# Optimization experiments

Measured on AMD Instinct MI355X. Metric: run time of the kernel, lower is better.

Reference implementation:

```python
import jax, jax.numpy as jnp
import numpy as np
import math

B, T, D, M, V = 16, 256, 256, 32, 50257
EPS = 1e-6


def setup_inputs() -> dict:
    key = jax.random.key(0)
    ks = jax.random.split(key, 24)
    s = 0.02
    inp = {
        'hidden_state': jax.random.normal(ks[0], (B, 2, D), jnp.float32),
        'output_sequence': jax.random.randint(ks[1], (B, T), 0, V),
        # embedding table for output tokens
        'emb_out': jax.random.normal(ks[2], (V, D), jnp.float32) * s,
        # decoder_attention (Wq,Wk,Wv are torch Linear weights [out,in], plus biases)
        'Wq1': jax.random.normal(ks[3], (D, D), jnp.float32) * s,
        'bq1': jnp.zeros((D,), jnp.float32),
        'Wk1': jax.random.normal(ks[4], (D, D), jnp.float32) * s,
        'bk1': jnp.zeros((D,), jnp.float32),
        'Wv1': jax.random.normal(ks[5], (D, D), jnp.float32) * s,
        'bv1': jnp.zeros((D,), jnp.float32),
        # decoder_attention_2
        'Wq2': jax.random.normal(ks[6], (D, D), jnp.float32) * s,
        'bq2': jnp.zeros((D,), jnp.float32),
        'Wk2': jax.random.normal(ks[7], (D, D), jnp.float32) * s,
        'bk2': jnp.zeros((D,), jnp.float32),
        'Wv2': jax.random.normal(ks[8], (D, D), jnp.float32) * s,
        'bv2': jnp.zeros((D,), jnp.float32),
        # decoder_mover / decoder_mover_2 weights: nn.Linear(D, M).weight -> [M, D]
        'mover1': jax.random.normal(ks[9], (M, D), jnp.float32) * s,
        'mover2': jax.random.normal(ks[10], (M, D), jnp.float32) * s,
        # norm2
        'gamma': jnp.ones((D,), jnp.float32),
        'beta': jnp.zeros((D,), jnp.float32),
        # vocab logits linear [V, D] + bias
        'Wvoc': jax.random.normal(ks[11], (V, D), jnp.float32) * s,
        'bvoc': jnp.zeros((V,), jnp.float32),
    }
    return inp


def _attn(q, kv, Wq, bq, Wk, bk, Wv, bv):
    # q: [B,1,D], kv: [B,M+1,D]
    Q = q @ Wq.T + bq
    K = kv @ Wk.T + bk
    Vv = kv @ Wv.T + bv
    s = jnp.einsum('bqd,bkd->bqk', Q, K) / jnp.sqrt(jnp.asarray(Q.shape[-1], Q.dtype))
    a = jax.nn.softmax(s, axis=-1)
    return jnp.einsum('bqk,bkd->bqd', a, Vv)


def _layernorm(x, gamma, beta):
    mu = jnp.mean(x, axis=-1, keepdims=True)
    var = jnp.mean((x - mu) ** 2, axis=-1, keepdims=True)
    return (x - mu) * jax.lax.rsqrt(var + EPS) * gamma + beta


def reference(hidden_state, output_sequence, emb_out,
              Wq1, bq1, Wk1, bk1, Wv1, bv1,
              Wq2, bq2, Wk2, bk2, Wv2, bv2,
              mover1, mover2, gamma, beta, Wvoc, bvoc):
    d = emb_out.shape[1]
    # Embeddings: lookup scaled by sqrt(d) (standard simple-transformer embedding)
    x = emb_out[output_sequence] * jnp.sqrt(jnp.asarray(d, jnp.float32))  # [B,T,D]
    z0 = hidden_state[:, 0:1, :]
    z1 = hidden_state[:, 1:2, :]
    b = z0.shape[0]
    mv1 = jnp.broadcast_to(mover1[None], (b, mover1.shape[0], d))  # static per step
    mv2 = jnp.broadcast_to(mover2[None], (b, mover2.shape[0], d))

    def step(carry, xt):
        z0, z1 = carry
        z0 = z0 + xt[:, None, :]
        g = jnp.concatenate([z0, mv1], axis=1)          # [B,M+1,D]
        dg = _attn(g[:, :1], g, Wq1, bq1, Wk1, bk1, Wv1, bv1)
        g2 = jnp.concatenate([z1, mv2], axis=1)
        dg2 = _attn(g2[:, :1], g2, Wq2, bq2, Wk2, bk2, Wv2, bv2)
        z0 = _layernorm(z0 + dg + dg2, gamma, beta)
        return (z0, z0), None

    (z0, z1), _ = jax.lax.scan(step, (z0, z1), jnp.swapaxes(x, 0, 1))
    logits = z0 @ Wvoc.T + bvoc                         # [B,1,V]
    y = jax.nn.log_softmax(logits, axis=-1)
    return jnp.concatenate([z0, z1], axis=1), y
```

## Files before the change

### kernel.cpp

```cpp
#include <hip/hip_runtime.h>

typedef unsigned int u32;
typedef unsigned short u16;

#define DD 256
#define TT 256
#define MM 32
#define NBATCH 16
#define VV 50257

#define WS_FLAG   0
#define WS_KV     16
#define WS_A      32784
#define WS_W12S   163856
#define WS_CB     180240
#define WS_E12    180752
#define WS_CST    180816
#define WS_ZFIN   180832
#define WS_SSUM   184928
#define WS_WPK    184944
#define WS_US     332400
#define WS_SYNC   369264

#if defined(__has_builtin)
#if __has_builtin(__builtin_amdgcn_fdot2)
#define HAS_FDOT2 1
#endif
#endif

typedef _Float16 half2_t __attribute__((ext_vector_type(2)));

__device__ __forceinline__ float bf2f(u16 v){ return __uint_as_float(((u32)v) << 16); }
__device__ __forceinline__ float ldf(const void* p, size_t i, int bf){
  return bf ? bf2f(((const u16*)p)[i]) : ((const float*)p)[i];
}
__device__ __forceinline__ u32 packh2(float a, float b){
  union { half2_t h; u32 u; } x;
  x.h[0] = (_Float16)a; x.h[1] = (_Float16)b;
  return x.u;
}
__device__ __forceinline__ float fdot2(u32 a, u32 b, float c){
  union { u32 u; half2_t h; } ua, ub;
  ua.u = a; ub.u = b;
#ifdef HAS_FDOT2
  return __builtin_amdgcn_fdot2(ua.h, ub.h, c, false);
#else
  return c + (float)ua.h[0]*(float)ub.h[0] + (float)ua.h[1]*(float)ub.h[1];
#endif
}
__device__ __forceinline__ u32 ldu(const u32* p){
  return __hip_atomic_load(p, __ATOMIC_RELAXED, __HIP_MEMORY_SCOPE_SYSTEM);
}
__device__ __forceinline__ void stu(u32* p, u32 v){
  __hip_atomic_store(p, v, __ATOMIC_RELAXED, __HIP_MEMORY_SCOPE_SYSTEM);
}
__device__ __forceinline__ void stv_tag(float* p, float v, u32 tag){
  stu((u32*)p, (__float_as_uint(v) & ~1u) | tag);
}

__global__ __launch_bounds__(256) void k_init(const u32* gam, u32* flag,
                                              float* Ssum, u32* sync, u32* usg){
  const int gtid = blockIdx.x*256 + threadIdx.x;
  if (blockIdx.x == 0){
    if (threadIdx.x == 0) *flag = (gam[0] == 0x3F800000u) ? 0u : 1u;
    if (threadIdx.x < 16) Ssum[threadIdx.x] = 0.f;
    for (int i = threadIdx.x; i < 512; i += 256) sync[i] = 0u;
  }
  for (int i = gtid; i < NBATCH*2304; i += 8*256) stu(&usg[i], 1u);
}

__global__ __launch_bounds__(256) void k_prep1(
  const void* Wk1, const void* bk1, const void* Wv1, const void* bv1,
  const void* Wk2, const void* bk2, const void* Wv2, const void* bv2,
  const void* m1, const void* m2, float* KV, const u32* flagp)
{
  const int bf = (int)*flagp;
  int mat = blockIdx.x >> 5, j = blockIdx.x & 31, d = threadIdx.x;
  const void *W, *bias, *mv;
  if (mat == 0){ W = Wk1; bias = bk1; mv = m1; }
  else if (mat == 1){ W = Wv1; bias = bv1; mv = m1; }
  else if (mat == 2){ W = Wk2; bias = bk2; mv = m2; }
  else { W = Wv2; bias = bv2; mv = m2; }
  float acc = ldf(bias, d, bf);
  for (int e = 0; e < DD; ++e) acc += ldf(W, d*DD + e, bf) * ldf(mv, j*DD + e, bf);
  KV[mat*8192 + j*DD + d] = acc;
}

__global__ __launch_bounds__(256) void k_prep2(
  const void* Wq1, const void* Wk1, const void* bq1, const void* bk1,
  const void* Wq2, const void* Wk2, const void* bq2, const void* bk2,
  const float* KV, float* A, float* W12s, float* cb, float* e12, float* cst,
  const u32* flagp)
{
  const int bf = (int)*flagp;
  int blk = blockIdx.x, tid = threadIdx.x;
  if (blk < 512){
    int mat = blk >> 8, i = blk & 255;
    const void* Wq = mat ? Wq2 : Wq1;
    const void* Wk = mat ? Wk2 : Wk1;
    float acc = 0.f;
    for (int e = 0; e < DD; ++e) acc += ldf(Wq, e*DD + i, bf) * ldf(Wk, e*DD + tid, bf);
    A[mat*65536 + i*DD + tid] = acc;
  } else if (blk < 576){
    int idx = blk - 512, mat = idx >> 5, j = idx & 31;
    const void* Wq = mat ? Wq2 : Wq1;
    const float* K = KV + mat*16384;
    float acc = 0.f;
    for (int e = 0; e < DD; ++e) acc += ldf(Wq, e*DD + tid, bf) * K[j*DD + e];
    W12s[mat*8192 + j*DD + tid] = acc;
  } else if (blk < 578){
    int mat = blk - 576;
    const void* Wq = mat ? Wq2 : Wq1;
    const void* Wk = mat ? Wk2 : Wk1;
    const void* bq = mat ? bq2 : bq1;
    const void* bk = mat ? bk2 : bk1;
    float acc = 0.f;
    for (int e = 0; e < DD; ++e)
      acc += ldf(Wk, e*DD + tid, bf) * ldf(bq, e, bf) + ldf(Wq, e*DD + tid, bf) * ldf(bk, e, bf);
    cb[mat*DD + tid] = acc;
  } else {
    if (tid < 32){
      float acc = 0.f;
      for (int d = 0; d < DD; ++d) acc += ldf(bq1, d, bf) * KV[tid*DD + d];
      e12[tid] = acc;
    } else if (tid < 64){
      int j = tid - 32; float acc = 0.f;
      for (int d = 0; d < DD; ++d) acc += ldf(bq2, d, bf) * KV[16384 + j*DD + d];
      e12[32 + j] = acc;
    } else if (tid == 64){
      float acc = 0.f;
      for (int d = 0; d < DD; ++d) acc += ldf(bq1, d, bf) * ldf(bk1, d, bf);
      cst[0] = acc;
    } else if (tid == 65){
      float acc = 0.f;
      for (int d = 0; d < DD; ++d) acc += ldf(bq2, d, bf) * ldf(bk2, d, bf);
      cst[1] = acc;
    }
  }
}

__global__ __launch_bounds__(256) void k_pack(
  const float* __restrict__ A, const float* __restrict__ W12s,
  const float* __restrict__ cb, const void* __restrict__ Wv1,
  const void* __restrict__ Wv2, u32* __restrict__ Wpk, const u32* flagp)
{
  const int bf = (int)*flagp;
  int idx = blockIdx.x*256 + threadIdx.x;
  float v0 = 0.f, v1 = 0.f;
  if (idx < 131072){
    int p = idx >> 15;
    int r2 = idx & 32767;
    int e2g = r2 >> 10;
    int t = (r2 >> 2) & 255;
    int q = r2 & 3;
    int c = e2g*8 + q*2;
    if (p == 0){ v0 = A[t*DD + c]; v1 = A[t*DD + c + 1]; }
    else if (p == 1){ v0 = ldf(Wv1, t*DD + c, bf); v1 = ldf(Wv1, t*DD + c + 1, bf); }
    else if (p == 2){ v0 = A[65536 + t*DD + c]; v1 = A[65536 + t*DD + c + 1]; }
    else { v0 = ldf(Wv2, t*DD + c, bf); v1 = ldf(Wv2, t*DD + c + 1, bf); }
  } else {
    int rem = idx - 131072;
    int t = rem >> 7;
    int e2g = (rem >> 2) & 31;
    int q = rem & 3;
    int c = e2g*8 + q*2;
    if (t < 32){ v0 = W12s[t*DD + c]; v1 = W12s[t*DD + c + 1]; }
    else if (t < 64){ v0 = W12s[8192 + (t-32)*DD + c]; v1 = W12s[8192 + (t-32)*DD + c + 1]; }
    else if (t == 64){ v0 = cb[c]; v1 = cb[c + 1]; }
    else if (t == 65){ v0 = cb[DD + c]; v1 = cb[DD + c + 1]; }
  }
  Wpk[idx] = packh2(v0, v1);
}

__global__ __launch_bounds__(256) void k_seq(
    const void* __restrict__ hid, const int* __restrict__ seq,
    const void* __restrict__ emb,
    const u32* __restrict__ Wpk, const float* __restrict__ V1g,
    const float* __restrict__ V2g, const float* __restrict__ e1g,
    const float* __restrict__ e2g_, const float* __restrict__ cst,
    const void* __restrict__ bv1, const void* __restrict__ bv2,
    const void* __restrict__ gam, const void* __restrict__ bet,
    float* __restrict__ zfin, float* __restrict__ out0,
    const u32* __restrict__ flagp, float* __restrict__ usg,
    u32* __restrict__ syncg)
{
  (void)syncg;
  __shared__ float z0s[DD], z1s[DD];
  __shared__ __align__(16) u32 zp0[128], zp1[128];
  __shared__ u32 V1h[MM*DD/2], V2h[MM*DD/2];
  __shared__ float a1s[33], a2s[33];
  __shared__ float red[16];
  __shared__ float gs[DD], bs[DD], bv1s[DD], bv2s[DD];
  __shared__ float e1s[MM], e2s[MM];
  __shared__ int toks[TT];

  const int tid = threadIdx.x;
  const int wg = blockIdx.x;
  const int b = wg >> 2;
  const int g = wg & 3;
  const int lane = tid & 63;
  const int wv = tid >> 6;
  const int bf = (int)*flagp;

  float* us0 = usg + b*2304;
  float* us1 = us0 + 1152;

  for (int r = tid; r < MM*DD/2; r += 256){
    V1h[r] = packh2(V1g[2*r], V1g[2*r + 1]);
    V2h[r] = packh2(V2g[2*r], V2g[2*r + 1]);
  }
  for (int r = tid; r < TT; r += 256) toks[r] = seq[b*TT + r];
  gs[tid] = ldf(gam, tid, bf); bs[tid] = ldf(bet, tid, bf);
  bv1s[tid] = ldf(bv1, tid, bf); bv2s[tid] = ldf(bv2, tid, bf);
  if (tid < MM){ e1s[tid] = e1g[tid]; e2s[tid] = e2g_[tid]; }
  const float c1 = cst[0], c2 = cst[1];
  __syncthreads();
  z1s[tid] = ldf(hid, b*2*DD + DD + tid, bf);
  z0s[tid] = ldf(hid, b*2*DD + tid, bf) + ldf(emb, (size_t)toks[0]*DD + tid, bf) * 16.0f;
  __syncthreads();

  const uint4* Wp = (const uint4*)Wpk;
  const uint4* wpMain = Wp + g*8192 + tid;
  const int p4row = g*32 + (tid >> 3);
  const uint4* wpP4 = Wp + 32768 + p4row*32 + (tid & 7);
  const bool p4z1 = (p4row >= 32 && p4row < 64) || (p4row == 65);

  int xi;
  if (tid < 2) xi = 1088 + tid;
  else if (tid >= 64 && tid < 128) xi = 1024 + (tid - 64);
  else xi = tid;

  for (int t = 0; t < TT; ++t){
    float* usw = (t & 1) ? us1 : us0;
    const u32 tg = (u32)((t >> 1) & 1);
    float xnext = 0.f;
    if (t + 1 < TT) xnext = ldf(emb, (size_t)toks[t+1]*DD + tid, bf) * 16.0f;

    if (tid < 128) zp0[tid] = packh2(z0s[2*tid], z0s[2*tid+1]);
    else { int i = tid - 128; zp1[i] = packh2(z1s[2*i], z1s[2*i+1]); }
    __syncthreads();

    {
      const uint4* zp4 = (const uint4*)((g < 2) ? zp0 : zp1);
      float a0 = 0.f, a1 = 0.f, a2 = 0.f, a3 = 0.f;
      #pragma unroll 8
      for (int k = 0; k < 32; ++k){
        uint4 w = wpMain[k*256];
        uint4 z = zp4[k];
        a0 = fdot2(w.x, z.x, a0);
        a1 = fdot2(w.y, z.y, a1);
        a2 = fdot2(w.z, z.z, a2);
        a3 = fdot2(w.w, z.w, a3);
      }
      stv_tag(&usw[g*256 + tid], (a0 + a1) + (a2 + a3), tg);
    }
    {
      const uint4* zq = (const uint4*)(p4z1 ? zp1 : zp0);
      float a0 = 0.f, a1 = 0.f, a2 = 0.f, a3 = 0.f;
      #pragma unroll
      for (int j = 0; j < 4; ++j){
        uint4 w = wpP4[j*8];
        uint4 z = zq[(tid & 7) + 8*j];
        a0 = fdot2(w.x, z.x, a0);
        a1 = fdot2(w.y, z.y, a1);
        a2 = fdot2(w.z, z.z, a2);
        a3 = fdot2(w.w, z.w, a3);
      }
      float s = (a0 + a1) + (a2 + a3);
      s += __shfl_down(s, 4, 64);
      s += __shfl_down(s, 2, 64);
      s += __shfl_down(s, 1, 64);
      if ((tid & 7) == 0) stv_tag(&usw[1024 + p4row], s, tg);
    }

    u32 b0, b1, b2, b3, bx;
    {
      const u32* up = (const u32*)usw;
      for (;;){
        b0 = ldu(up + tid);
        b1 = ldu(up + 256 + tid);
        b2 = ldu(up + 512 + tid);
        b3 = ldu(up + 768 + tid);
        bx = ldu(up + xi);
        if ((((b0 ^ tg) | (b1 ^ tg) | (b2 ^ tg) | (b3 ^ tg) | (bx ^ tg)) & 1u) == 0u)
          break;
      }
    }
    float u0  = __uint_as_float(b0);
    float uv1 = __uint_as_float(b1);
    float u2  = __uint_as_float(b2);
    float uv2 = __uint_as_float(b3);
    float xf  = __uint_as_float(bx);

    float p1 = z0s[tid] * u0;
    float p2 = z1s[tid] * u2;
    #pragma unroll
    for (int off = 32; off; off >>= 1){
      p1 += __shfl_down(p1, off, 64);
      p2 += __shfl_down(p2, off, 64);
    }
    if (lane == 0){ red[wv] = p1; red[4 + wv] = p2; }
    __syncthreads();
    if (tid == 0) a1s[0] = (red[0]+red[1]+red[2]+red[3] + xf + c1) * 0.0625f;
    if (tid == 1) a2s[0] = (red[4]+red[5]+red[6]+red[7] + xf + c2) * 0.0625f;
    if (tid >= 64 && tid < 96)  a1s[tid - 63] = (xf + e1s[tid-64]) * 0.0625f;
    if (tid >= 96 && tid < 128) a2s[tid - 95] = (xf + e2s[tid-96]) * 0.0625f;
    __syncthreads();

    if (tid < 128){
      float* sm = (tid < 64) ? a1s : a2s;
      float v = (lane < 33) ? sm[lane] : -1e30f;
      float mx = v;
      #pragma unroll
      for (int off = 32; off; off >>= 1) mx = fmaxf(mx, __shfl_xor(mx, off, 64));
      float e = (lane < 33) ? expf(v - mx) : 0.f;
      float s = e;
      #pragma unroll
      for (int off = 32; off; off >>= 1) s += __shfl_xor(s, off, 64);
      if (lane < 33) sm[lane] = e / s;
    }
    __syncthreads();

    float hv1 = uv1 + bv1s[tid];
    float hv2 = uv2 + bv2s[tid];
    float dg = a1s[0] * hv1;
    float dh = a2s[0] * hv2;
    int half_idx = tid >> 1;
    #pragma unroll
    for (int j = 1; j <= 32; ++j){
      union { u32 u; half2_t h; } pv1, pv2;
      pv1.u = V1h[((j-1) << 7) + half_idx];
      pv2.u = V2h[((j-1) << 7) + half_idx];
      float e1v = (tid & 1) ? (float)pv1.h[1] : (float)pv1.h[0];
      float e2v = (tid & 1) ? (float)pv2.h[1] : (float)pv2.h[0];
      dg += a1s[j] * e1v;
      dh += a2s[j] * e2v;
    }
    float y = z0s[tid] + dg + dh;
    float sy = y, syy = y * y;
    #pragma unroll
    for (int off = 32; off; off >>= 1){
      sy += __shfl_down(sy, off, 64);
      syy += __shfl_down(syy, off, 64);
    }
    if (lane == 0){ red[8 + wv] = sy; red[12 + wv] = syy; }
    __syncthreads();
    float Sy = red[8] + red[9] + red[10] + red[11];
    float Syy = red[12] + red[13] + red[14] + red[15];
    float mu = Sy * (1.f/DD);
    float var = Syy * (1.f/DD) - mu*mu;
    float zi = (y - mu) * rsqrtf(var + 1e-6f) * gs[tid] + bs[tid];
    if (t == TT - 1){
      if (g == 0){
        zfin[b*DD + tid] = zi;
        out0[b*2*DD + tid] = zi;
        out0[b*2*DD + DD + tid] = zi;
      }
    } else {
      z1s[tid] = zi;
      z0s[tid] = zi + xnext;
    }
    __syncthreads();
  }
}

__global__ __launch_bounds__(256) void k_logits(
    const float* __restrict__ zfin, const void* __restrict__ Wvoc,
    const void* __restrict__ bvoc, float* __restrict__ Ssum,
    float* __restrict__ out1, const u32* __restrict__ flagp)
{
  __shared__ float zfs[NBATCH][DD];
  const int tid = threadIdx.x;
  const int bf = (int)*flagp;
  for (int r = tid; r < NBATCH*DD; r += 256) zfs[r >> 8][r & 255] = zfin[r];
  __syncthreads();

  const int v = blockIdx.x*256 + tid;
  float acc[NBATCH];
  const bool ok = (v < VV);
  float bias = ok ? ldf(bvoc, v, bf) : 0.f;
  #pragma unroll
  for (int b = 0; b < NBATCH; ++b) acc[b] = bias;

  if (ok){
    if (bf){
      const uint4* wr = ((const uint4*)Wvoc) + (size_t)v*32;
      for (int gg = 0; gg < 32; ++gg){
        uint4 u = wr[gg];
        float w0 = __uint_as_float(u.x << 16), w1 = __uint_as_float(u.x & 0xffff0000u);
        float w2 = __uint_as_float(u.y << 16), w3 = __uint_as_float(u.y & 0xffff0000u);
        float w4 = __uint_as_float(u.z << 16), w5 = __uint_as_float(u.z & 0xffff0000u);
        float w6 = __uint_as_float(u.w << 16), w7 = __uint_as_float(u.w & 0xffff0000u);
        const int c = gg*8;
        #pragma unroll
        for (int b = 0; b < NBATCH; ++b){
          const float* zc = &zfs[b][c];
          acc[b] += w0*zc[0] + w1*zc[1] + w2*zc[2] + w3*zc[3]
                  + w4*zc[4] + w5*zc[5] + w6*zc[6] + w7*zc[7];
        }
      }
    } else {
      const float4* wr = ((const float4*)Wvoc) + (size_t)v*64;
      for (int gg = 0; gg < 64; ++gg){
        float4 u = wr[gg];
        const int c = gg*4;
        #pragma unroll
        for (int b = 0; b < NBATCH; ++b){
          const float* zc = &zfs[b][c];
          acc[b] += u.x*zc[0] + u.y*zc[1] + u.z*zc[2] + u.w*zc[3];
        }
      }
    }
    #pragma unroll
    for (int b = 0; b < NBATCH; ++b) out1[(size_t)b*VV + v] = acc[b];
  }

  #pragma unroll
  for (int b = 0; b < NBATCH; ++b){
    float p = ok ? expf(acc[b]) : 0.f;
    #pragma unroll
    for (int off = 32; off; off >>= 1) p += __shfl_down(p, off, 64);
    if ((tid & 63) == 0) atomicAdd(&Ssum[b], p);
  }
}

__global__ __launch_bounds__(256) void k_final(
    const float* __restrict__ Ssum, float* __restrict__ out1)
{
  const int v = blockIdx.x*256 + threadIdx.x;
  const int b = blockIdx.y;
  if (v < VV){
    float ls = logf(Ssum[b]);
    size_t i = (size_t)b*VV + v;
    out1[i] = out1[i] - ls;
  }
}

extern "C" void kernel_launch(void* const* d_in, const int* in_sizes, int n_in,
                              void* d_out, int out_size, void* d_ws, size_t ws_size,
                              hipStream_t stream)
{
  (void)in_sizes; (void)n_in; (void)out_size; (void)ws_size;
  const void* hid  = d_in[0];
  const int*  seq  = (const int*)d_in[1];
  const void* emb  = d_in[2];
  const void* Wq1  = d_in[3];
  const void* bq1  = d_in[4];
  const void* Wk1  = d_in[5];
  const void* bk1  = d_in[6];
  const void* Wv1  = d_in[7];
  const void* bv1  = d_in[8];
  const void* Wq2  = d_in[9];
  const void* bq2  = d_in[10];
  const void* Wk2  = d_in[11];
  const void* bk2  = d_in[12];
  const void* Wv2  = d_in[13];
  const void* bv2  = d_in[14];
  const void* m1   = d_in[15];
  const void* m2   = d_in[16];
  const void* gam  = d_in[17];
  const void* bet  = d_in[18];
  const void* Wvoc = d_in[19];
  const void* bvoc = d_in[20];

  float* wsf    = (float*)d_ws;
  u32*   flag   = (u32*)(wsf + WS_FLAG);
  float* KV     = wsf + WS_KV;
  float* A      = wsf + WS_A;
  float* W12s   = wsf + WS_W12S;
  float* cb     = wsf + WS_CB;
  float* e12    = wsf + WS_E12;
  float* cst    = wsf + WS_CST;
  float* zfin   = wsf + WS_ZFIN;
  float* Ssum   = wsf + WS_SSUM;
  u32*   Wpk    = (u32*)(wsf + WS_WPK);
  float* usg    = wsf + WS_US;
  u32*   syncg  = (u32*)(wsf + WS_SYNC);

  float* out0 = (float*)d_out;
  float* out1 = out0 + NBATCH*2*DD;

  k_init<<<8, 256, 0, stream>>>((const u32*)gam, flag, Ssum, syncg, (u32*)usg);
  k_prep1<<<128, 256, 0, stream>>>(Wk1,bk1,Wv1,bv1,Wk2,bk2,Wv2,bv2,m1,m2,KV,flag);
  k_prep2<<<579, 256, 0, stream>>>(Wq1,Wk1,bq1,bk1,Wq2,Wk2,bq2,bk2,KV,A,W12s,cb,e12,cst,flag);
  k_pack<<<576, 256, 0, stream>>>(A,W12s,cb,Wv1,Wv2,Wpk,flag);
  k_seq<<<NBATCH*4, 256, 0, stream>>>(hid, seq, emb, Wpk, KV+8192, KV+24576,
                                      e12, e12+32, cst, bv1, bv2, gam, bet, zfin, out0,
                                      flag, usg, syncg);
  k_logits<<<197, 256, 0, stream>>>(zfin, Wvoc, bvoc, Ssum, out1, flag);
  k_final<<<dim3(197, NBATCH), 256, 0, stream>>>(Ssum, out1);
}
```

Measured before the change: 1.788 ms.

## Map batch groups to same XCD and use agent-scope atomics when co-located

Reorders the block-to-(batch,group) mapping so the four cooperating workgroups of a batch are blockIdx b, b+16, b+32, b+48, which with round-robin XCD dispatch likely places them on the same XCD. At startup each group reads its XCC_ID via s_getreg and publishes it. If all four match, the per-step exchange of tagged partial results uses agent-scope rather than system-scope atomic loads and stores, which is meant to cut the cost of cross-workgroup handoffs in the 256-step sequential loop. It adds a startup handshake and relies on the hardware dispatch order. It also stores a sentinel into the exchange buffers after the loop, and sync is now zeroed with system-scope stores.

```diff
diff --git a/kernel.cpp b/kernel.cpp
--- a/kernel.cpp
+++ b/kernel.cpp
@@ -48,14 +48,26 @@
   return c + (float)ua.h[0]*(float)ub.h[0] + (float)ua.h[1]*(float)ub.h[1];
 #endif
 }
+
 __device__ __forceinline__ u32 ldu(const u32* p){
   return __hip_atomic_load(p, __ATOMIC_RELAXED, __HIP_MEMORY_SCOPE_SYSTEM);
 }
 __device__ __forceinline__ void stu(u32* p, u32 v){
   __hip_atomic_store(p, v, __ATOMIC_RELAXED, __HIP_MEMORY_SCOPE_SYSTEM);
 }
-__device__ __forceinline__ void stv_tag(float* p, float v, u32 tag){
-  stu((u32*)p, (__float_as_uint(v) & ~1u) | tag);
+template<bool FAST>
+__device__ __forceinline__ u32 ldx(const u32* p){
+  return __hip_atomic_load(p, __ATOMIC_RELAXED,
+      FAST ? __HIP_MEMORY_SCOPE_AGENT : __HIP_MEMORY_SCOPE_SYSTEM);
+}
+template<bool FAST>
+__device__ __forceinline__ void stx(u32* p, u32 v){
+  __hip_atomic_store(p, v, __ATOMIC_RELAXED,
+      FAST ? __HIP_MEMORY_SCOPE_AGENT : __HIP_MEMORY_SCOPE_SYSTEM);
+}
+template<bool FAST>
+__device__ __forceinline__ void stx_tag(float* p, float v, u32 tag){
+  stx<FAST>((u32*)p, (__float_as_uint(v) & ~1u) | tag);
 }
 
 __global__ __launch_bounds__(256) void k_init(const u32* gam, u32* flag,
@@ -64,7 +76,7 @@
   if (blockIdx.x == 0){
     if (threadIdx.x == 0) *flag = (gam[0] == 0x3F800000u) ? 0u : 1u;
     if (threadIdx.x < 16) Ssum[threadIdx.x] = 0.f;
-    for (int i = threadIdx.x; i < 512; i += 256) sync[i] = 0u;
+    for (int i = threadIdx.x; i < 512; i += 256) stu(&sync[i], 0u);
   }
   for (int i = gtid; i < NBATCH*2304; i += 8*256) stu(&usg[i], 1u);
 }
@@ -172,64 +184,19 @@
   Wpk[idx] = packh2(v0, v1);
 }
 
-__global__ __launch_bounds__(256) void k_seq(
-    const void* __restrict__ hid, const int* __restrict__ seq,
-    const void* __restrict__ emb,
-    const u32* __restrict__ Wpk, const float* __restrict__ V1g,
-    const float* __restrict__ V2g, const float* __restrict__ e1g,
-    const float* __restrict__ e2g_, const float* __restrict__ cst,
-    const void* __restrict__ bv1, const void* __restrict__ bv2,
-    const void* __restrict__ gam, const void* __restrict__ bet,
-    float* __restrict__ zfin, float* __restrict__ out0,
-    const u32* __restrict__ flagp, float* __restrict__ usg,
-    u32* __restrict__ syncg)
-{
-  (void)syncg;
-  __shared__ float z0s[DD], z1s[DD];
-  __shared__ __align__(16) u32 zp0[128], zp1[128];
-  __shared__ u32 V1h[MM*DD/2], V2h[MM*DD/2];
-  __shared__ float a1s[33], a2s[33];
-  __shared__ float red[16];
-  __shared__ float gs[DD], bs[DD], bv1s[DD], bv2s[DD];
-  __shared__ float e1s[MM], e2s[MM];
-  __shared__ int toks[TT];
-
-  const int tid = threadIdx.x;
-  const int wg = blockIdx.x;
-  const int b = wg >> 2;
-  const int g = wg & 3;
-  const int lane = tid & 63;
-  const int wv = tid >> 6;
-  const int bf = (int)*flagp;
-
-  float* us0 = usg + b*2304;
-  float* us1 = us0 + 1152;
-
-  for (int r = tid; r < MM*DD/2; r += 256){
-    V1h[r] = packh2(V1g[2*r], V1g[2*r + 1]);
-    V2h[r] = packh2(V2g[2*r], V2g[2*r + 1]);
-  }
-  for (int r = tid; r < TT; r += 256) toks[r] = seq[b*TT + r];
-  gs[tid] = ldf(gam, tid, bf); bs[tid] = ldf(bet, tid, bf);
-  bv1s[tid] = ldf(bv1, tid, bf); bv2s[tid] = ldf(bv2, tid, bf);
-  if (tid < MM){ e1s[tid] = e1g[tid]; e2s[tid] = e2g_[tid]; }
-  const float c1 = cst[0], c2 = cst[1];
-  __syncthreads();
-  z1s[tid] = ldf(hid, b*2*DD + DD + tid, bf);
-  z0s[tid] = ldf(hid, b*2*DD + tid, bf) + ldf(emb, (size_t)toks[0]*DD + tid, bf) * 16.0f;
-  __syncthreads();
-
-  const uint4* Wp = (const uint4*)Wpk;
-  const uint4* wpMain = Wp + g*8192 + tid;
-  const int p4row = g*32 + (tid >> 3);
-  const uint4* wpP4 = Wp + 32768 + p4row*32 + (tid & 7);
-  const bool p4z1 = (p4row >= 32 && p4row < 64) || (p4row == 65);
-
-  int xi;
-  if (tid < 2) xi = 1088 + tid;
-  else if (tid >= 64 && tid < 128) xi = 1024 + (tid - 64);
-  else xi = tid;
-
+template<bool FAST>
+__device__ __forceinline__ void seq_loop(
+    int tid, int g, int b, int lane, int wv, int bf,
+    float* us0, float* us1,
+    const uint4* wpMain, const uint4* wpP4, bool p4z1, int p4row, int xi,
+    const void* emb, const int* toks, float c1, float c2,
+    float* z0s, float* z1s, u32* zp0, u32* zp1,
+    const u32* V1h, const u32* V2h,
+    float* a1s, float* a2s, float* red,
+    const float* gs, const float* bs, const float* bv1s, const float* bv2s,
+    const float* e1s, const float* e2s,
+    float* zfin, float* out0)
+{
   for (int t = 0; t < TT; ++t){
     float* usw = (t & 1) ? us1 : us0;
     const u32 tg = (u32)((t >> 1) & 1);
@@ -252,7 +219,7 @@
         a2 = fdot2(w.z, z.z, a2);
         a3 = fdot2(w.w, z.w, a3);
       }
-      stv_tag(&usw[g*256 + tid], (a0 + a1) + (a2 + a3), tg);
+      stx_tag<FAST>(&usw[g*256 + tid], (a0 + a1) + (a2 + a3), tg);
     }
     {
       const uint4* zq = (const uint4*)(p4z1 ? zp1 : zp0);
@@ -270,18 +237,18 @@
       s += __shfl_down(s, 4, 64);
       s += __shfl_down(s, 2, 64);
       s += __shfl_down(s, 1, 64);
-      if ((tid & 7) == 0) stv_tag(&usw[1024 + p4row], s, tg);
+      if ((tid & 7) == 0) stx_tag<FAST>(&usw[1024 + p4row], s, tg);
     }
 
     u32 b0, b1, b2, b3, bx;
     {
       const u32* up = (const u32*)usw;
       for (;;){
-        b0 = ldu(up + tid);
-        b1 = ldu(up + 256 + tid);
-        b2 = ldu(up + 512 + tid);
-        b3 = ldu(up + 768 + tid);
-        bx = ldu(up + xi);
+        b0 = ldx<FAST>(up + tid);
+        b1 = ldx<FAST>(up + 256 + tid);
+        b2 = ldx<FAST>(up + 512 + tid);
+        b3 = ldx<FAST>(up + 768 + tid);
+        bx = ldx<FAST>(up + xi);
         if ((((b0 ^ tg) | (b1 ^ tg) | (b2 ^ tg) | (b3 ^ tg) | (bx ^ tg)) & 1u) == 0u)
           break;
       }
@@ -321,8 +288,9 @@
     }
     __syncthreads();
 
-    float hv1 = uv1 + bv1s[tid];
+    float hv1 = __uint_as_float(b1) + bv1s[tid];
     float hv2 = uv2 + bv2s[tid];
+    (void)uv1;
     float dg = a1s[0] * hv1;
     float dh = a2s[0] * hv2;
     int half_idx = tid >> 1;
@@ -362,6 +330,96 @@
     }
     __syncthreads();
   }
+
+  const u32 P = 0x7fffffffu;
+  stx<FAST>((u32*)&us0[g*256 + tid], P);
+  stx<FAST>((u32*)&us1[g*256 + tid], P);
+  if ((tid & 7) == 0){
+    stx<FAST>((u32*)&us0[1024 + p4row], P);
+    stx<FAST>((u32*)&us1[1024 + p4row], P);
+  }
+}
+
+__global__ __launch_bounds__(256) void k_seq(
+    const void* __restrict__ hid, const int* __restrict__ seq,
+    const void* __restrict__ emb,
+    const u32* __restrict__ Wpk, const float* __restrict__ V1g,
+    const float* __restrict__ V2g, const float* __restrict__ e1g,
+    const float* __restrict__ e2g_, const float* __restrict__ cst,
+    const void* __restrict__ bv1, const void* __restrict__ bv2,
+    const void* __restrict__ gam, const void* __restrict__ bet,
+    float* __restrict__ zfin, float* __restrict__ out0,
+    const u32* __restrict__ flagp, float* __restrict__ usg,
+    u32* __restrict__ syncg)
+{
+  __shared__ float z0s[DD], z1s[DD];
+  __shared__ __align__(16) u32 zp0[128], zp1[128];
+  __shared__ u32 V1h[MM*DD/2], V2h[MM*DD/2];
+  __shared__ float a1s[33], a2s[33];
+  __shared__ float red[16];
+  __shared__ float gs[DD], bs[DD], bv1s[DD], bv2s[DD];
+  __shared__ float e1s[MM], e2s[MM];
+  __shared__ int toks[TT];
+  __shared__ u32 fastsh;
+
+  const int tid = threadIdx.x;
+  const int wg = blockIdx.x;
+  const int b = wg & 15;
+  const int g = wg >> 4;
+  const int lane = tid & 63;
+  const int wv = tid >> 6;
+  const int bf = (int)*flagp;
+
+  float* us0 = usg + b*2304;
+  float* us1 = us0 + 1152;
+  u32* det = syncg + b*8;
+
+  u32 myxcd = 0;
+  asm volatile("s_getreg_b32 %0, hwreg(HW_REG_XCC_ID)" : "=s"(myxcd));
+  if (tid == 0){
+    stu(&det[g], myxcd + 1u);
+    u32 v0, v1, v2, v3;
+    do {
+      v0 = ldu(&det[0]); v1 = ldu(&det[1]);
+      v2 = ldu(&det[2]); v3 = ldu(&det[3]);
+    } while (!(v0 && v1 && v2 && v3));
+    fastsh = (v0 == v1 && v1 == v2 && v2 == v3) ? 1u : 0u;
+  }
+
+  for (int r = tid; r < MM*DD/2; r += 256){
+    V1h[r] = packh2(V1g[2*r], V1g[2*r + 1]);
+    V2h[r] = packh2(V2g[2*r], V2g[2*r + 1]);
+  }
+  for (int r = tid; r < TT; r += 256) toks[r] = seq[b*TT + r];
+  gs[tid] = ldf(gam, tid, bf); bs[tid] = ldf(bet, tid, bf);
+  bv1s[tid] = ldf(bv1, tid, bf); bv2s[tid] = ldf(bv2, tid, bf);
+  if (tid < MM){ e1s[tid] = e1g[tid]; e2s[tid] = e2g_[tid]; }
+  const float c1 = cst[0], c2 = cst[1];
+  __syncthreads();
+  z1s[tid] = ldf(hid, b*2*DD + DD + tid, bf);
+  z0s[tid] = ldf(hid, b*2*DD + tid, bf) + ldf(emb, (size_t)toks[0]*DD + tid, bf) * 16.0f;
+  const bool fast = (fastsh != 0);
+  __syncthreads();
+
+  const uint4* Wp = (const uint4*)Wpk;
+  const uint4* wpMain = Wp + g*8192 + tid;
+  const int p4row = g*32 + (tid >> 3);
+  const uint4* wpP4 = Wp + 32768 + p4row*32 + (tid & 7);
+  const bool p4z1 = (p4row >= 32 && p4row < 64) || (p4row == 65);
+
+  int xi;
+  if (tid < 2) xi = 1088 + tid;
+  else if (tid >= 64 && tid < 128) xi = 1024 + (tid - 64);
+  else xi = tid;
+
+  if (fast)
+    seq_loop<true >(tid, g, b, lane, wv, bf, us0, us1, wpMain, wpP4, p4z1, p4row, xi,
+                    emb, toks, c1, c2, z0s, z1s, zp0, zp1, V1h, V2h, a1s, a2s, red,
+                    gs, bs, bv1s, bv2s, e1s, e2s, zfin, out0);
+  else
+    seq_loop<false>(tid, g, b, lane, wv, bf, us0, us1, wpMain, wpP4, p4z1, p4row, xi,
+                    emb, toks, c1, c2, z0s, z1s, zp0, zp1, V1h, V2h, a1s, a2s, red,
+                    gs, bs, bv1s, bv2s, e1s, e2s, zfin, out0);
 }
 
 __global__ __launch_bounds__(256) void k_logits(
```

After: 1.758 ms. No clear change (-1.7%).
